# Kernel tuning notes

Hardware: AMD Instinct MI355X
Metric: run time of the kernel (lower is better)

## Reference

```python
import jax, jax.numpy as jnp
import numpy as np

T, B, E, H = 2048, 2, 1024, 16
Dh = E // H


def setup_inputs() -> dict:
    key = jax.random.key(0)
    ks = jax.random.split(key, 5)
    s = 0.02
    query = jax.random.normal(ks[0], (T, B, E), dtype=jnp.float32)
    Wq = jax.random.normal(ks[1], (E, E), dtype=jnp.float32) * s
    Wk = jax.random.normal(ks[2], (E, E), dtype=jnp.float32) * s
    Wv = jax.random.normal(ks[3], (E, E), dtype=jnp.float32) * s
    Wo = jax.random.normal(ks[4], (E, E), dtype=jnp.float32) * s
    bq = jnp.zeros((E,), jnp.float32)
    bk = jnp.zeros((E,), jnp.float32)
    bv = jnp.zeros((E,), jnp.float32)
    bo = jnp.zeros((E,), jnp.float32)
    # additive causal mask: 0 on/below diagonal, -inf above (standard fairseq usage)
    neg = jnp.finfo(jnp.float32).min
    attn_mask = jnp.where(jnp.triu(jnp.ones((T, T), jnp.bool_), k=1), neg, 0.0).astype(jnp.float32)
    return {"query": query, "Wq": Wq, "bq": bq, "Wk": Wk, "bk": bk,
            "Wv": Wv, "bv": bv, "Wo": Wo, "bo": bo, "attn_mask": attn_mask}


def reference(query, Wq, bq, Wk, bk, Wv, bv, Wo, bo, attn_mask):
    t, b, e = query.shape
    scale = Dh ** -0.5
    # self-attention projections (nn.Linear: x @ W.T + b)
    q = (query @ Wq.T + bq) * scale  # [T,B,E]
    k = query @ Wk.T + bk
    v = query @ Wv.T + bv
    # [T, B*H, Dh] -> [B*H, T, Dh]
    q = q.reshape(t, b * H, Dh).transpose(1, 0, 2)
    k = k.reshape(t, b * H, Dh).transpose(1, 0, 2)
    v = v.reshape(t, b * H, Dh).transpose(1, 0, 2)
    # explicit bmm -> softmax -> bmm (materializes [B*H, T, T])
    attn_weights = jnp.einsum('btd,bsd->bts', q, k) + attn_mask[None, :, :]
    attn_probs = jax.nn.softmax(attn_weights, axis=-1)
    attn = jnp.einsum('bts,bsd->btd', attn_probs, v)  # [B*H, T, Dh]
    attn = attn.transpose(1, 0, 2).reshape(t, b, e)  # [T,B,E]
    out = attn @ Wo.T + bo
    return out
```

## Files before the change

kernel.cpp:

```cpp
#include <hip/hip_runtime.h>


typedef __attribute__((ext_vector_type(8))) short   s16x8;
typedef __attribute__((ext_vector_type(4))) float   f32x4;
typedef __attribute__((ext_vector_type(2))) __fp16  f16x2;
typedef __attribute__((ext_vector_type(4))) __fp16  f16x4;

#define MFMA16(a, b, c) __builtin_amdgcn_mfma_f32_16x16x32_bf16((a), (b), (c), 0, 0, 0)
#define MFMApv(a, b, c) __builtin_amdgcn_mfma_f32_16x16x16f16((a), (b), (c), 0, 0, 0)

static __device__ __forceinline__ unsigned short f2bf(float f) {
    unsigned u = __float_as_uint(f);
    unsigned r = u + 0x7fffu + ((u >> 16) & 1u);
    return (unsigned short)(r >> 16);
}

static __device__ __forceinline__ void gl2lds16(const void* g, void* l) {
    __builtin_amdgcn_global_load_lds(
        (const __attribute__((address_space(1))) unsigned int*)g,
        (__attribute__((address_space(3))) unsigned int*)l, 16, 0, 0);
}

__global__ __launch_bounds__(256) void cvt_all(const float* __restrict__ query,
                                               const float* __restrict__ w0,
                                               const float* __restrict__ w1,
                                               const float* __restrict__ w2,
                                               const float* __restrict__ w3,
                                               unsigned short* __restrict__ Xb,
                                               unsigned short* __restrict__ Wcat) {
    const int bx = blockIdx.x;
    if (bx < 4096) {
        const int i = threadIdx.x;
        const float4 f = reinterpret_cast<const float4*>(query + (size_t)bx * 1024)[i];
        ushort4 u;
        u.x = f2bf(f.x); u.y = f2bf(f.y); u.z = f2bf(f.z); u.w = f2bf(f.w);
        const int mrow = (bx & 1) * 2048 + (bx >> 1);
        reinterpret_cast<ushort4*>(Xb + (size_t)mrow * 1024)[i] = u;
    } else {
        const int j   = bx - 4096;
        const int sel = j >> 10;
        const int i   = (j & 1023) * 256 + threadIdx.x;
        const float* src = (sel == 0) ? w0 : (sel == 1) ? w1 : (sel == 2) ? w2 : w3;
        const float4 f = reinterpret_cast<const float4*>(src)[i];
        ushort4 u;
        u.x = f2bf(f.x); u.y = f2bf(f.y); u.z = f2bf(f.z); u.w = f2bf(f.w);
        reinterpret_cast<ushort4*>(Wcat + (size_t)sel * 1048576)[i] = u;
    }
}

__global__ __launch_bounds__(512, 2) void gemm_qkv(const unsigned short* __restrict__ A,
                                                   const unsigned short* __restrict__ W,
                                                   const float* __restrict__ b0,
                                                   const float* __restrict__ b1,
                                                   const float* __restrict__ b2,
                                                   unsigned short* __restrict__ outQK,
                                                   __fp16* __restrict__ outV) {
    __shared__ __align__(16) unsigned short smem[57344];

    const int tid  = threadIdx.x;
    const int w    = tid >> 6;
    const int lane = tid & 63;
    const int quad = lane >> 4;
    const int c    = lane & 15;
    const int wm   = w >> 2;
    const int wn   = w & 3;

    const int id   = blockIdx.x;
    const int xcd  = id & 7;
    const int slot = id >> 3;
    const int m0 = (xcd * 2 + (slot & 1)) * 256;
    const int n0 = (slot >> 1) * 192;

    f32x4 acc[8][3];
    #pragma unroll
    for (int mi = 0; mi < 8; ++mi)
        #pragma unroll
        for (int ni = 0; ni < 3; ++ni) acc[mi][ni] = (f32x4){0.f, 0.f, 0.f, 0.f};

    const int srow = tid >> 3;
    const int g    = (tid & 7) ^ (srow & 7);
    const unsigned short* aG = A + (size_t)(m0 + srow) * 1024 + g * 8;
    const unsigned short* wG = W + (size_t)(n0 + srow) * 1024 + g * 8;
    const int loff = tid * 8;

#define STA(buf, u, k0) gl2lds16(aG + (k0) + (u) * 65536, &smem[(buf) * 28672 + (u) * 4096 + loff])
#define STB(buf, u, k0) gl2lds16(wG + (k0) + (u) * 65536, &smem[(buf) * 28672 + 16384 + (u) * 4096 + loff])

    STB(0, 0, 0); STB(0, 1, 0); STB(0, 2, 0);
    STA(0, 0, 0); STA(0, 2, 0); STA(0, 1, 0); STA(0, 3, 0);
    asm volatile("s_waitcnt vmcnt(2)" ::: "memory");
    asm volatile("s_barrier" ::: "memory");

    const int cs  = c & 7;
    const int ch0 = (quad ^ cs) << 3;
    const int ch1 = ((4 + quad) ^ cs) << 3;

    s16x8 af[4][2], bf[3][2];

    #pragma unroll
    for (int mi = 0; mi < 4; ++mi) {
        const int row = (wm * 128 + mi * 16 + c) * 64;
        af[mi][0] = *reinterpret_cast<const s16x8*>(&smem[row + ch0]);
        af[mi][1] = *reinterpret_cast<const s16x8*>(&smem[row + ch1]);
    }
    #pragma unroll
    for (int ni = 0; ni < 3; ++ni) {
        const int row = (wn * 48 + ni * 16 + c) * 64;
        bf[ni][0] = *reinterpret_cast<const s16x8*>(&smem[16384 + row + ch0]);
        bf[ni][1] = *reinterpret_cast<const s16x8*>(&smem[16384 + row + ch1]);
    }

    #pragma unroll 1
    for (int t = 0; t < 16; ++t) {
        const unsigned short* Al = &smem[(t & 1) * 28672];
        const int  nb   = (t & 1) ^ 1;
        const int  kn   = (t + 1) * 64;
        const bool more = (t < 15);

        if (more) {
            STB(nb, 0, kn); STB(nb, 1, kn); STB(nb, 2, kn);
            STA(nb, 0, kn); STA(nb, 2, kn); STA(nb, 1, kn); STA(nb, 3, kn);
        }

        __builtin_amdgcn_s_setprio(1);
        #pragma unroll
        for (int mi = 0; mi < 4; ++mi)
            #pragma unroll
            for (int ni = 0; ni < 3; ++ni) {
                acc[mi][ni] = MFMA16(af[mi][0], bf[ni][0], acc[mi][ni]);
                acc[mi][ni] = MFMA16(af[mi][1], bf[ni][1], acc[mi][ni]);
            }
        __builtin_amdgcn_s_setprio(0);

        if (more) asm volatile("s_waitcnt vmcnt(7)" ::: "memory");
        else      asm volatile("s_waitcnt vmcnt(0)" ::: "memory");
        asm volatile("s_barrier" ::: "memory");

        #pragma unroll
        for (int mi = 0; mi < 4; ++mi) {
            const int row = (wm * 128 + 64 + mi * 16 + c) * 64;
            af[mi][0] = *reinterpret_cast<const s16x8*>(&Al[row + ch0]);
            af[mi][1] = *reinterpret_cast<const s16x8*>(&Al[row + ch1]);
        }
        __builtin_amdgcn_s_setprio(1);
        #pragma unroll
        for (int mi = 0; mi < 4; ++mi)
            #pragma unroll
            for (int ni = 0; ni < 3; ++ni) {
                acc[4 + mi][ni] = MFMA16(af[mi][0], bf[ni][0], acc[4 + mi][ni]);
                acc[4 + mi][ni] = MFMA16(af[mi][1], bf[ni][1], acc[4 + mi][ni]);
            }
        __builtin_amdgcn_s_setprio(0);

        if (more) {
            asm volatile("s_waitcnt vmcnt(2)" ::: "memory");
            asm volatile("s_barrier" ::: "memory");
            const unsigned short* An = &smem[nb * 28672];
            #pragma unroll
            for (int mi = 0; mi < 4; ++mi) {
                const int row = (wm * 128 + mi * 16 + c) * 64;
                af[mi][0] = *reinterpret_cast<const s16x8*>(&An[row + ch0]);
                af[mi][1] = *reinterpret_cast<const s16x8*>(&An[row + ch1]);
            }
            #pragma unroll
            for (int ni = 0; ni < 3; ++ni) {
                const int row = (wn * 48 + ni * 16 + c) * 64;
                bf[ni][0] = *reinterpret_cast<const s16x8*>(&An[16384 + row + ch0]);
                bf[ni][1] = *reinterpret_cast<const s16x8*>(&An[16384 + row + ch1]);
            }
        }
    }
#undef STA
#undef STB

    const float qs = 0.18033688011112042f;
    #pragma unroll
    for (int ni = 0; ni < 3; ++ni) {
        const int n = n0 + wn * 48 + ni * 16 + c;
        if (n < 2048) {
            const float bval  = (n < 1024) ? b0[n] : b1[n & 1023];
            const float scale = (n < 1024) ? qs : 1.0f;
            #pragma unroll
            for (int mi = 0; mi < 8; ++mi)
                #pragma unroll
                for (int r = 0; r < 4; ++r) {
                    const int m = m0 + wm * 128 + mi * 16 + quad * 4 + r;
                    outQK[(size_t)m * 2048 + n] = f2bf((acc[mi][ni][r] + bval) * scale);
                }
        }
    }

    if (n0 >= 1920) {
        const int vg0 = (n0 >= 2048) ? (n0 - 2048) : 0;
        const int nV  = n0 + 192 - ((n0 > 2048) ? n0 : 2048);
        __fp16* lds16 = reinterpret_cast<__fp16*>(smem);
        __syncthreads();
        #pragma unroll
        for (int ni = 0; ni < 3; ++ni) {
            const int n = n0 + wn * 48 + ni * 16 + c;
            if (n >= 2048) {
                const int lv = (n - 2048) - vg0;
                const float bval = b2[n - 2048];
                #pragma unroll
                for (int mi = 0; mi < 8; ++mi) {
                    const int m = wm * 128 + mi * 16 + quad * 4;
                    const f16x2 lo = __builtin_amdgcn_cvt_pkrtz(acc[mi][ni][0] + bval,
                                                                acc[mi][ni][1] + bval);
                    const f16x2 hi = __builtin_amdgcn_cvt_pkrtz(acc[mi][ni][2] + bval,
                                                                acc[mi][ni][3] + bval);
                    uint2 st;
                    st.x = __builtin_bit_cast(unsigned int, lo);
                    st.y = __builtin_bit_cast(unsigned int, hi);
                    const int phys = lv * 256 + (((m >> 3) ^ (lv & 31)) << 3) + (m & 7);
                    *reinterpret_cast<uint2*>(&lds16[phys]) = st;
                }
            }
        }
        __syncthreads();
        const int lv = tid >> 1;
        if (lv < nV) {
            const int vcol = vg0 + lv;
            const int bb = m0 >> 11, tbase = m0 & 2047;
            __fp16* vdst = outV + ((size_t)((bb * 16 + (vcol >> 6)) * 64 + (vcol & 63))) * 2048 + tbase;
            #pragma unroll
            for (int j = 0; j < 16; ++j) {
                const int lc = (tid & 1) * 16 + j;
                *reinterpret_cast<uint4*>(vdst + lc * 8) =
                    *reinterpret_cast<const uint4*>(&lds16[lv * 256 + ((lc ^ (lv & 31)) << 3)]);
            }
        }
    }
}

__global__ __launch_bounds__(256) void gemm_out(const unsigned short* __restrict__ A,
                                                const unsigned short* __restrict__ W,
                                                const float* __restrict__ bias,
                                                float* __restrict__ outF) {
    __shared__ __align__(16) unsigned short Al[2][64 * 64];
    __shared__ __align__(16) unsigned short Bl[2][128 * 64];

    const int tid  = threadIdx.x;
    const int w    = tid >> 6;
    const int lane = tid & 63;
    const int quad = lane >> 4;
    const int c    = lane & 15;

    const int id   = blockIdx.x;
    const int xcd  = id & 7;
    const int slot = id >> 3;
    const int m0 = (xcd * 8 + (slot & 7)) * 64;
    const int n0 = (slot >> 3) * 128;

    f32x4 acc[8];
    #pragma unroll
    for (int ni = 0; ni < 8; ++ni) acc[ni] = (f32x4){0.f, 0.f, 0.f, 0.f};

    const int srow = tid >> 3;
    const int g    = (tid & 7) ^ (srow & 7);
    const unsigned short* aG = A + (size_t)(m0 + srow) * 1024 + g * 8;
    const unsigned short* wG = W + (size_t)(n0 + srow) * 1024 + g * 8;
    const int loff = tid * 8;

    const int cs = (c & 7);

    gl2lds16(aG,             &Al[0][loff]);
    gl2lds16(aG + 32 * 1024, &Al[0][loff + 2048]);
    #pragma unroll
    for (int i = 0; i < 4; ++i)
        gl2lds16(wG + i * 32 * 1024, &Bl[0][loff + i * 2048]);

    #pragma unroll 1
    for (int kk = 0; kk < 16; ++kk) {
        __syncthreads();
        if (kk < 15) {
            const int k0n = (kk + 1) * 64;
            const int nb  = (kk + 1) & 1;
            gl2lds16(aG + k0n,             &Al[nb][loff]);
            gl2lds16(aG + k0n + 32 * 1024, &Al[nb][loff + 2048]);
            #pragma unroll
            for (int i = 0; i < 4; ++i)
                gl2lds16(wG + k0n + i * 32 * 1024, &Bl[nb][loff + i * 2048]);
        }
        const int cb = kk & 1;
        const int arow = (w * 16 + c) * 64;
        const s16x8 af0 = *reinterpret_cast<const s16x8*>(&Al[cb][arow + ((quad ^ cs) << 3)]);
        const s16x8 af1 = *reinterpret_cast<const s16x8*>(&Al[cb][arow + (((4 + quad) ^ cs) << 3)]);
        __builtin_amdgcn_s_setprio(1);
        #pragma unroll
        for (int ni = 0; ni < 8; ++ni) {
            const int brow = (ni * 16 + c) * 64;
            const s16x8 bf0 = *reinterpret_cast<const s16x8*>(&Bl[cb][brow + ((quad ^ cs) << 3)]);
            const s16x8 bf1 = *reinterpret_cast<const s16x8*>(&Bl[cb][brow + (((4 + quad) ^ cs) << 3)]);
            acc[ni] = MFMA16(af0, bf0, acc[ni]);
            acc[ni] = MFMA16(af1, bf1, acc[ni]);
        }
        __builtin_amdgcn_s_setprio(0);
    }

    #pragma unroll
    for (int ni = 0; ni < 8; ++ni) {
        const int n = n0 + ni * 16 + c;
        const float bval = bias[n];
        const int m = m0 + w * 16 + quad * 4;
        const int bb = m >> 11, t = m & 2047;
        #pragma unroll
        for (int r = 0; r < 4; ++r)
            outF[(size_t)(2 * (t + r) + bb) * 1024 + n] = acc[ni][r] + bval;
    }
}

__global__ __launch_bounds__(256, 4) void attn_kernel(const unsigned short* __restrict__ QKb,
                                                      const __fp16* __restrict__ Vt,
                                                      unsigned short* __restrict__ Ob) {
    __shared__ unsigned short Kl[2][2][64][32];
    __shared__ __fp16 Vl[2][64][64];

    const int tid  = threadIdx.x;
    const int w    = tid >> 6;
    const int lane = tid & 63;
    const int quad = lane >> 4;
    const int c    = lane & 15;

    const int id = blockIdx.x;
    const int bh = (id & 7) * 4 + ((id >> 3) & 3);
    const int kidx = id >> 5;
    const int rr   = kidx >> 3, jj = kidx & 7;
    const int a    = (rr & 1) ? (24 - 8 * rr + jj) : (31 - 8 * rr - jj);
    const int bB = bh >> 4, h = bh & 15;
    const int t0 = a * 64;
    const int trg = t0 + w * 16;
    const int nIt = a + 1;

    const unsigned short* qp = QKb + (size_t)(bB * 2048 + trg + c) * 2048 + h * 64 + quad * 8;
    const s16x8 aq0 = *reinterpret_cast<const s16x8*>(qp);
    const s16x8 aq1 = *reinterpret_cast<const s16x8*>(qp + 32);

    const int lr4 = lane >> 2, sl4 = lane & 3;
    const unsigned short* kSrc = QKb + (size_t)(bB * 2048 + w * 16 + lr4) * 2048
                                 + 1024 + h * 64 + (sl4 ^ ((lane >> 3) & 3)) * 8;
    const int vr8 = lane >> 3, sl8 = lane & 7;
    const __fp16* vSrcA = Vt + (size_t)(bh * 64 + w * 16 + vr8) * 2048 + (sl8 ^ vr8) * 8;
    const __fp16* vSrcB = vSrcA + (size_t)8 * 2048;

    f32x4 acc[4];
    float l = 0.f;
    #pragma unroll
    for (int dt = 0; dt < 4; ++dt) acc[dt] = (f32x4){0.f, 0.f, 0.f, 0.f};

    const int kswz = (quad ^ ((c >> 1) & 3)) * 8;

    {
        gl2lds16(kSrc,      &Kl[0][0][w * 16 + lr4][sl4 * 8]);
        gl2lds16(kSrc + 32, &Kl[0][1][w * 16 + lr4][sl4 * 8]);
        gl2lds16(vSrcA,     &Vl[0][w * 16 + vr8][sl8 * 8]);
        gl2lds16(vSrcB,     &Vl[0][w * 16 + 8 + vr8][sl8 * 8]);
    }

    for (int it = 0; it < nIt; ++it) {
        const int buf = it & 1;
        __syncthreads();
        if (it + 1 < nIt) {
            const size_t s1 = (size_t)(it + 1) * 64;
            const int nb = buf ^ 1;
            gl2lds16(kSrc + s1 * 2048,      &Kl[nb][0][w * 16 + lr4][sl4 * 8]);
            gl2lds16(kSrc + s1 * 2048 + 32, &Kl[nb][1][w * 16 + lr4][sl4 * 8]);
            gl2lds16(vSrcA + s1,            &Vl[nb][w * 16 + vr8][sl8 * 8]);
            gl2lds16(vSrcB + s1,            &Vl[nb][w * 16 + 8 + vr8][sl8 * 8]);
        }

        s16x8 kf[4][2];
        #pragma unroll
        for (int ns = 0; ns < 4; ++ns) {
            kf[ns][0] = *reinterpret_cast<const s16x8*>(&Kl[buf][0][ns * 16 + c][kswz]);
            kf[ns][1] = *reinterpret_cast<const s16x8*>(&Kl[buf][1][ns * 16 + c][kswz]);
        }
        f16x4 vf[4][4];
        #pragma unroll
        for (int dt = 0; dt < 4; ++dt)
            #pragma unroll
            for (int ch = 0; ch < 4; ++ch) {
                const int phys = ((2 * ch + (quad >> 1)) ^ (c & 7)) * 8 + (quad & 1) * 4;
                vf[dt][ch] = *reinterpret_cast<const f16x4*>(&Vl[buf][dt * 16 + c][phys]);
            }

        const int s0 = it * 64;
        const bool diag = (it == a);
        f32x4 sT[4];
        __builtin_amdgcn_s_setprio(1);
        #pragma unroll
        for (int ns = 0; ns < 4; ++ns) {
            f32x4 z = (f32x4){0.f, 0.f, 0.f, 0.f};
            z = MFMA16(kf[ns][0], aq0, z);
            sT[ns] = MFMA16(kf[ns][1], aq1, z);
        }
        __builtin_amdgcn_s_setprio(0);
        f16x4 pf[4];
        float lp = 0.f;
        #pragma unroll
        for (int ns = 0; ns < 4; ++ns) {
            float pv[4];
            #pragma unroll
            for (int r = 0; r < 4; ++r) pv[r] = __builtin_amdgcn_exp2f(sT[ns][r]);
            if (diag) {
                const int sb = s0 + ns * 16 + quad * 4;
                const int qg = trg + c;
                #pragma unroll
                for (int r = 0; r < 4; ++r) if (sb + r > qg) pv[r] = 0.f;
            }
            lp += (pv[0] + pv[1]) + (pv[2] + pv[3]);
            const f16x2 lo = __builtin_amdgcn_cvt_pkrtz(pv[0], pv[1]);
            const f16x2 hi = __builtin_amdgcn_cvt_pkrtz(pv[2], pv[3]);
            pf[ns] = __builtin_shufflevector(lo, hi, 0, 1, 2, 3);
        }
        l += lp;
        __builtin_amdgcn_s_setprio(1);
        #pragma unroll
        for (int dt = 0; dt < 4; ++dt)
            #pragma unroll
            for (int ns = 0; ns < 4; ++ns)
                acc[dt] = MFMApv(vf[dt][ns], pf[ns], acc[dt]);
        __builtin_amdgcn_s_setprio(0);
    }

    float lv = l;
    lv += __shfl_xor(lv, 16);
    lv += __shfl_xor(lv, 32);
    const float inv = 1.0f / lv;
    const size_t base = (size_t)(bB * 2048 + trg + c) * 1024 + h * 64;
    #pragma unroll
    for (int dt = 0; dt < 4; ++dt) {
        const unsigned u0 = (unsigned)f2bf(acc[dt][0] * inv)
                          | ((unsigned)f2bf(acc[dt][1] * inv) << 16);
        const unsigned u1 = (unsigned)f2bf(acc[dt][2] * inv)
                          | ((unsigned)f2bf(acc[dt][3] * inv) << 16);
        uint2 st; st.x = u0; st.y = u1;
        *reinterpret_cast<uint2*>(Ob + base + dt * 16 + quad * 4) = st;
    }
}

extern "C" void kernel_launch(void* const* d_in, const int* in_sizes, int n_in,
                              void* d_out, int out_size, void* d_ws, size_t ws_size,
                              hipStream_t stream) {
    const float* query = (const float*)d_in[0];
    const float* Wq    = (const float*)d_in[1];
    const float* bq    = (const float*)d_in[2];
    const float* Wk    = (const float*)d_in[3];
    const float* bk    = (const float*)d_in[4];
    const float* Wv    = (const float*)d_in[5];
    const float* bv    = (const float*)d_in[6];
    const float* Wo    = (const float*)d_in[7];
    const float* bo    = (const float*)d_in[8];

    float* out = (float*)d_out;

    unsigned short* ws    = (unsigned short*)d_ws;
    unsigned short* Xbf   = ws;
    unsigned short* Wcat  = Xbf  + (size_t)4096 * 1024;
    unsigned short* QKb   = Wcat + (size_t)4 * 1024 * 1024;
    __fp16*         Vtw   = (__fp16*)(QKb + (size_t)4096 * 2048);
    unsigned short* attnb = (unsigned short*)(Vtw + (size_t)32 * 64 * 2048);

    cvt_all<<<8192, 256, 0, stream>>>(query, Wq, Wk, Wv, Wo, Xbf, Wcat);

    gemm_qkv<<<256, 512, 0, stream>>>(Xbf, Wcat, bq, bk, bv, QKb, Vtw);

    attn_kernel<<<1024, 256, 0, stream>>>(QKb, Vtw, attnb);

    gemm_out<<<512, 256, 0, stream>>>(attnb, Wcat + (size_t)3 * 1024 * 1024,
                                      bo, out);
}
```

Baseline: 187.3 us.

## Double query rows per attention block to reuse K/V tiles across two row groups

Each attention block now covers 128 query rows instead of 64, with every wave handling two 16-row groups that share the same K and V fragments loaded from LDS. The grid is halved and launch bounds drop to 2 blocks per SM. The aim is to halve K/V global and LDS traffic per query row and amortise the loop overhead. The cost is more registers per thread (two accumulator sets), lower occupancy, coarser causal work balance, and an extra diagonal tile computed for the first row group.

```diff
diff --git a/kernel.cpp b/kernel.cpp
--- a/kernel.cpp
+++ b/kernel.cpp
@@ -309,7 +309,7 @@
     }
 }
 
-__global__ __launch_bounds__(256, 4) void attn_kernel(const unsigned short* __restrict__ QKb,
+__global__ __launch_bounds__(256, 2) void attn_kernel(const unsigned short* __restrict__ QKb,
                                                       const __fp16* __restrict__ Vt,
                                                       unsigned short* __restrict__ Ob) {
     __shared__ unsigned short Kl[2][2][64][32];
@@ -324,16 +324,18 @@
     const int id = blockIdx.x;
     const int bh = (id & 7) * 4 + ((id >> 3) & 3);
     const int kidx = id >> 5;
-    const int rr   = kidx >> 3, jj = kidx & 7;
-    const int a    = (rr & 1) ? (24 - 8 * rr + jj) : (31 - 8 * rr - jj);
+    const int a    = (kidx < 8) ? (15 - kidx) : (kidx - 8);
     const int bB = bh >> 4, h = bh & 15;
-    const int t0 = a * 64;
-    const int trg = t0 + w * 16;
-    const int nIt = a + 1;
-
-    const unsigned short* qp = QKb + (size_t)(bB * 2048 + trg + c) * 2048 + h * 64 + quad * 8;
-    const s16x8 aq0 = *reinterpret_cast<const s16x8*>(qp);
-    const s16x8 aq1 = *reinterpret_cast<const s16x8*>(qp + 32);
+    const int t0 = a * 128;
+    const int trg = t0 + w * 32;
+    const int nIt = 2 * a + 2;
+
+    const unsigned short* qp0 = QKb + (size_t)(bB * 2048 + trg + c) * 2048 + h * 64 + quad * 8;
+    const s16x8 aq0 = *reinterpret_cast<const s16x8*>(qp0);
+    const s16x8 aq1 = *reinterpret_cast<const s16x8*>(qp0 + 32);
+    const unsigned short* qp1 = qp0 + (size_t)16 * 2048;
+    const s16x8 aq2 = *reinterpret_cast<const s16x8*>(qp1);
+    const s16x8 aq3 = *reinterpret_cast<const s16x8*>(qp1 + 32);
 
     const int lr4 = lane >> 2, sl4 = lane & 3;
     const unsigned short* kSrc = QKb + (size_t)(bB * 2048 + w * 16 + lr4) * 2048
@@ -342,10 +344,13 @@
     const __fp16* vSrcA = Vt + (size_t)(bh * 64 + w * 16 + vr8) * 2048 + (sl8 ^ vr8) * 8;
     const __fp16* vSrcB = vSrcA + (size_t)8 * 2048;
 
-    f32x4 acc[4];
-    float l = 0.f;
-    #pragma unroll
-    for (int dt = 0; dt < 4; ++dt) acc[dt] = (f32x4){0.f, 0.f, 0.f, 0.f};
+    f32x4 acc0[4], acc1[4];
+    float l0 = 0.f, l1 = 0.f;
+    #pragma unroll
+    for (int dt = 0; dt < 4; ++dt) {
+        acc0[dt] = (f32x4){0.f, 0.f, 0.f, 0.f};
+        acc1[dt] = (f32x4){0.f, 0.f, 0.f, 0.f};
+    }
 
     const int kswz = (quad ^ ((c >> 1) & 3)) * 8;
 
@@ -384,7 +389,7 @@
             }
 
         const int s0 = it * 64;
-        const bool diag = (it == a);
+
         f32x4 sT[4];
         __builtin_amdgcn_s_setprio(1);
         #pragma unroll
@@ -394,47 +399,96 @@
             sT[ns] = MFMA16(kf[ns][1], aq1, z);
         }
         __builtin_amdgcn_s_setprio(0);
-        f16x4 pf[4];
-        float lp = 0.f;
+        f16x4 pf0[4];
+        {
+            const bool dg = (s0 + 63 > trg);
+            float lp = 0.f;
+            #pragma unroll
+            for (int ns = 0; ns < 4; ++ns) {
+                float pv[4];
+                #pragma unroll
+                for (int r = 0; r < 4; ++r) pv[r] = __builtin_amdgcn_exp2f(sT[ns][r]);
+                if (dg) {
+                    const int sb = s0 + ns * 16 + quad * 4;
+                    const int qg = trg + c;
+                    #pragma unroll
+                    for (int r = 0; r < 4; ++r) if (sb + r > qg) pv[r] = 0.f;
+                }
+                lp += (pv[0] + pv[1]) + (pv[2] + pv[3]);
+                const f16x2 lo = __builtin_amdgcn_cvt_pkrtz(pv[0], pv[1]);
+                const f16x2 hi = __builtin_amdgcn_cvt_pkrtz(pv[2], pv[3]);
+                pf0[ns] = __builtin_shufflevector(lo, hi, 0, 1, 2, 3);
+            }
+            l0 += lp;
+        }
+
+        __builtin_amdgcn_s_setprio(1);
         #pragma unroll
         for (int ns = 0; ns < 4; ++ns) {
-            float pv[4];
-            #pragma unroll
-            for (int r = 0; r < 4; ++r) pv[r] = __builtin_amdgcn_exp2f(sT[ns][r]);
-            if (diag) {
-                const int sb = s0 + ns * 16 + quad * 4;
-                const int qg = trg + c;
+            f32x4 z = (f32x4){0.f, 0.f, 0.f, 0.f};
+            z = MFMA16(kf[ns][0], aq2, z);
+            sT[ns] = MFMA16(kf[ns][1], aq3, z);
+        }
+        __builtin_amdgcn_s_setprio(0);
+        f16x4 pf1[4];
+        {
+            const bool dg = (s0 + 63 > trg + 16);
+            float lp = 0.f;
+            #pragma unroll
+            for (int ns = 0; ns < 4; ++ns) {
+                float pv[4];
                 #pragma unroll
-                for (int r = 0; r < 4; ++r) if (sb + r > qg) pv[r] = 0.f;
-            }
-            lp += (pv[0] + pv[1]) + (pv[2] + pv[3]);
-            const f16x2 lo = __builtin_amdgcn_cvt_pkrtz(pv[0], pv[1]);
-            const f16x2 hi = __builtin_amdgcn_cvt_pkrtz(pv[2], pv[3]);
-            pf[ns] = __builtin_shufflevector(lo, hi, 0, 1, 2, 3);
-        }
-        l += lp;
+                for (int r = 0; r < 4; ++r) pv[r] = __builtin_amdgcn_exp2f(sT[ns][r]);
+                if (dg) {
+                    const int sb = s0 + ns * 16 + quad * 4;
+                    const int qg = trg + 16 + c;
+                    #pragma unroll
+                    for (int r = 0; r < 4; ++r) if (sb + r > qg) pv[r] = 0.f;
+                }
+                lp += (pv[0] + pv[1]) + (pv[2] + pv[3]);
+                const f16x2 lo = __builtin_amdgcn_cvt_pkrtz(pv[0], pv[1]);
+                const f16x2 hi = __builtin_amdgcn_cvt_pkrtz(pv[2], pv[3]);
+                pf1[ns] = __builtin_shufflevector(lo, hi, 0, 1, 2, 3);
+            }
+            l1 += lp;
+        }
+
         __builtin_amdgcn_s_setprio(1);
         #pragma unroll
         for (int dt = 0; dt < 4; ++dt)
             #pragma unroll
-            for (int ns = 0; ns < 4; ++ns)
-                acc[dt] = MFMApv(vf[dt][ns], pf[ns], acc[dt]);
+            for (int ns = 0; ns < 4; ++ns) {
+                acc0[dt] = MFMApv(vf[dt][ns], pf0[ns], acc0[dt]);
+                acc1[dt] = MFMApv(vf[dt][ns], pf1[ns], acc1[dt]);
+            }
         __builtin_amdgcn_s_setprio(0);
     }
 
-    float lv = l;
-    lv += __shfl_xor(lv, 16);
-    lv += __shfl_xor(lv, 32);
-    const float inv = 1.0f / lv;
-    const size_t base = (size_t)(bB * 2048 + trg + c) * 1024 + h * 64;
+    float lv0 = l0;
+    lv0 += __shfl_xor(lv0, 16);
+    lv0 += __shfl_xor(lv0, 32);
+    const float inv0 = 1.0f / lv0;
+    float lv1 = l1;
+    lv1 += __shfl_xor(lv1, 16);
+    lv1 += __shfl_xor(lv1, 32);
+    const float inv1 = 1.0f / lv1;
+
+    const size_t base0 = (size_t)(bB * 2048 + trg + c) * 1024 + h * 64;
+    const size_t base1 = base0 + (size_t)16 * 1024;
     #pragma unroll
     for (int dt = 0; dt < 4; ++dt) {
-        const unsigned u0 = (unsigned)f2bf(acc[dt][0] * inv)
-                          | ((unsigned)f2bf(acc[dt][1] * inv) << 16);
-        const unsigned u1 = (unsigned)f2bf(acc[dt][2] * inv)
-                          | ((unsigned)f2bf(acc[dt][3] * inv) << 16);
+        unsigned u0 = (unsigned)f2bf(acc0[dt][0] * inv0)
+                    | ((unsigned)f2bf(acc0[dt][1] * inv0) << 16);
+        unsigned u1 = (unsigned)f2bf(acc0[dt][2] * inv0)
+                    | ((unsigned)f2bf(acc0[dt][3] * inv0) << 16);
         uint2 st; st.x = u0; st.y = u1;
-        *reinterpret_cast<uint2*>(Ob + base + dt * 16 + quad * 4) = st;
+        *reinterpret_cast<uint2*>(Ob + base0 + dt * 16 + quad * 4) = st;
+        u0 = (unsigned)f2bf(acc1[dt][0] * inv1)
+           | ((unsigned)f2bf(acc1[dt][1] * inv1) << 16);
+        u1 = (unsigned)f2bf(acc1[dt][2] * inv1)
+           | ((unsigned)f2bf(acc1[dt][3] * inv1) << 16);
+        uint2 st2; st2.x = u0; st2.y = u1;
+        *reinterpret_cast<uint2*>(Ob + base1 + dt * 16 + quad * 4) = st2;
     }
 }
 
@@ -464,7 +518,7 @@
 
     gemm_qkv<<<256, 512, 0, stream>>>(Xbf, Wcat, bq, bk, bv, QKb, Vtw);
 
-    attn_kernel<<<1024, 256, 0, stream>>>(QKb, Vtw, attnb);
+    attn_kernel<<<512, 256, 0, stream>>>(QKb, Vtw, attnb);
 
     gemm_out<<<512, 256, 0, stream>>>(attnb, Wcat + (size_t)3 * 1024 * 1024,
                                       bo, out);
```

After: 205.6 us. +9.8%, slower.

## Split long causal attention rows across key chunks with a combine kernel

Applied to the files above, without the earlier changes.

Long query tiles now have their key range split into 2-4 chunks, each handled by a separate block, giving 2560 blocks instead of 1024 and work that is more evenly sized. Chunks write unnormalized fp32 partial outputs and row sums to workspace, and a new combine kernel adds them and normalizes. The aim is to remove the causal tail imbalance where a few blocks run many iterations. The cost is extra global traffic for the partials, plus an additional kernel launch. The split relies on a fixed max rather than per-chunk max tracking, as the original already did.

```diff
diff --git a/kernel.cpp b/kernel.cpp
--- a/kernel.cpp
+++ b/kernel.cpp
@@ -311,7 +311,9 @@
 
 __global__ __launch_bounds__(256, 4) void attn_kernel(const unsigned short* __restrict__ QKb,
                                                       const __fp16* __restrict__ Vt,
-                                                      unsigned short* __restrict__ Ob) {
+                                                      unsigned short* __restrict__ Ob,
+                                                      float* __restrict__ Po,
+                                                      float* __restrict__ Pl) {
     __shared__ unsigned short Kl[2][2][64][32];
     __shared__ __fp16 Vl[2][64][64];
 
@@ -322,14 +324,23 @@
     const int c    = lane & 15;
 
     const int id = blockIdx.x;
-    const int bh = (id & 7) * 4 + ((id >> 3) & 3);
-    const int kidx = id >> 5;
-    const int rr   = kidx >> 3, jj = kidx & 7;
-    const int a    = (rr & 1) ? (24 - 8 * rr + jj) : (31 - 8 * rr - jj);
+    const int bh = id & 31;
+    const int e  = 79 - (id >> 5);
+    int a, ci, nc;
+    if (e < 8)       { a = e;                ci = 0;          nc = 1; }
+    else if (e < 24) { const int k = e - 8;  a = 8 + (k >> 1);  ci = k & 1;      nc = 2; }
+    else if (e < 48) { const int k = e - 24; const int q3 = (k * 11) >> 5;
+                       a = 16 + q3;          ci = k - 3 * q3;  nc = 3; }
+    else             { const int k = e - 48; a = 24 + (k >> 2); ci = k & 3;      nc = 4; }
+    const int U = a + 1;
+    int u0, u1;
+    if (nc == 1)      { u0 = 0;                  u1 = U; }
+    else if (nc == 2) { u0 = (ci * U) >> 1;      u1 = ((ci + 1) * U) >> 1; }
+    else if (nc == 3) { u0 = (ci * U * 11) >> 5; u1 = ((ci + 1) * U * 11) >> 5; }
+    else              { u0 = (ci * U) >> 2;      u1 = ((ci + 1) * U) >> 2; }
+
     const int bB = bh >> 4, h = bh & 15;
-    const int t0 = a * 64;
-    const int trg = t0 + w * 16;
-    const int nIt = a + 1;
+    const int trg = a * 64 + w * 16;
 
     const unsigned short* qp = QKb + (size_t)(bB * 2048 + trg + c) * 2048 + h * 64 + quad * 8;
     const s16x8 aq0 = *reinterpret_cast<const s16x8*>(qp);
@@ -350,16 +361,18 @@
     const int kswz = (quad ^ ((c >> 1) & 3)) * 8;
 
     {
-        gl2lds16(kSrc,      &Kl[0][0][w * 16 + lr4][sl4 * 8]);
-        gl2lds16(kSrc + 32, &Kl[0][1][w * 16 + lr4][sl4 * 8]);
-        gl2lds16(vSrcA,     &Vl[0][w * 16 + vr8][sl8 * 8]);
-        gl2lds16(vSrcB,     &Vl[0][w * 16 + 8 + vr8][sl8 * 8]);
-    }
-
-    for (int it = 0; it < nIt; ++it) {
+        const size_t s0r = (size_t)u0 * 64;
+        const int b0 = u0 & 1;
+        gl2lds16(kSrc + s0r * 2048,      &Kl[b0][0][w * 16 + lr4][sl4 * 8]);
+        gl2lds16(kSrc + s0r * 2048 + 32, &Kl[b0][1][w * 16 + lr4][sl4 * 8]);
+        gl2lds16(vSrcA + s0r,            &Vl[b0][w * 16 + vr8][sl8 * 8]);
+        gl2lds16(vSrcB + s0r,            &Vl[b0][w * 16 + 8 + vr8][sl8 * 8]);
+    }
+
+    for (int it = u0; it < u1; ++it) {
         const int buf = it & 1;
         __syncthreads();
-        if (it + 1 < nIt) {
+        if (it + 1 < u1) {
             const size_t s1 = (size_t)(it + 1) * 64;
             const int nb = buf ^ 1;
             gl2lds16(kSrc + s1 * 2048,      &Kl[nb][0][w * 16 + lr4][sl4 * 8]);
@@ -425,16 +438,70 @@
     float lv = l;
     lv += __shfl_xor(lv, 16);
     lv += __shfl_xor(lv, 32);
-    const float inv = 1.0f / lv;
-    const size_t base = (size_t)(bB * 2048 + trg + c) * 1024 + h * 64;
-    #pragma unroll
-    for (int dt = 0; dt < 4; ++dt) {
-        const unsigned u0 = (unsigned)f2bf(acc[dt][0] * inv)
-                          | ((unsigned)f2bf(acc[dt][1] * inv) << 16);
-        const unsigned u1 = (unsigned)f2bf(acc[dt][2] * inv)
-                          | ((unsigned)f2bf(acc[dt][3] * inv) << 16);
-        uint2 st; st.x = u0; st.y = u1;
-        *reinterpret_cast<uint2*>(Ob + base + dt * 16 + quad * 4) = st;
+
+    if (nc == 1) {
+        const float inv = 1.0f / lv;
+        const size_t base = (size_t)(bB * 2048 + trg + c) * 1024 + h * 64;
+        #pragma unroll
+        for (int dt = 0; dt < 4; ++dt) {
+            const unsigned u0b = (unsigned)f2bf(acc[dt][0] * inv)
+                               | ((unsigned)f2bf(acc[dt][1] * inv) << 16);
+            const unsigned u1b = (unsigned)f2bf(acc[dt][2] * inv)
+                               | ((unsigned)f2bf(acc[dt][3] * inv) << 16);
+            uint2 st; st.x = u0b; st.y = u1b;
+            *reinterpret_cast<uint2*>(Ob + base + dt * 16 + quad * 4) = st;
+        }
+    } else {
+        const int slot = (bh * 32 + a) * 4 + ci;
+        float* po = Po + (size_t)slot * 4096 + (w * 16 + c) * 64 + quad * 4;
+        #pragma unroll
+        for (int dt = 0; dt < 4; ++dt) {
+            float4 st;
+            st.x = acc[dt][0]; st.y = acc[dt][1]; st.z = acc[dt][2]; st.w = acc[dt][3];
+            *reinterpret_cast<float4*>(po + dt * 16) = st;
+        }
+        if (quad == 0) Pl[(size_t)slot * 64 + w * 16 + c] = lv;
+    }
+}
+
+__global__ __launch_bounds__(256) void attn_combine(const float* __restrict__ Po,
+                                                    const float* __restrict__ Pl,
+                                                    unsigned short* __restrict__ Ob) {
+    const int id = blockIdx.x;
+    const int bh = id & 31;
+    const int a  = 8 + (id >> 5);
+    const int nc = (a < 16) ? 2 : (a < 24) ? 3 : 4;
+    const int bB = bh >> 4, h = bh & 15;
+
+    const int tid = threadIdx.x;
+    const int q   = tid >> 2;
+    const int ds  = (tid & 3) * 16;
+
+    const int slot0 = (bh * 32 + a) * 4;
+
+    float lsum = 0.f;
+    for (int ci = 0; ci < nc; ++ci) lsum += Pl[(size_t)(slot0 + ci) * 64 + q];
+    const float inv = 1.0f / lsum;
+
+    float4 o[4];
+    #pragma unroll
+    for (int j = 0; j < 4; ++j) o[j] = (float4){0.f, 0.f, 0.f, 0.f};
+    for (int ci = 0; ci < nc; ++ci) {
+        const float* p = Po + (size_t)(slot0 + ci) * 4096 + q * 64 + ds;
+        #pragma unroll
+        for (int j = 0; j < 4; ++j) {
+            const float4 v = reinterpret_cast<const float4*>(p)[j];
+            o[j].x += v.x; o[j].y += v.y; o[j].z += v.z; o[j].w += v.w;
+        }
+    }
+
+    unsigned short* dst = Ob + (size_t)(bB * 2048 + a * 64 + q) * 1024 + h * 64 + ds;
+    #pragma unroll
+    for (int j = 0; j < 4; ++j) {
+        uint2 st;
+        st.x = (unsigned)f2bf(o[j].x * inv) | ((unsigned)f2bf(o[j].y * inv) << 16);
+        st.y = (unsigned)f2bf(o[j].z * inv) | ((unsigned)f2bf(o[j].w * inv) << 16);
+        *reinterpret_cast<uint2*>(dst + j * 4) = st;
     }
 }
 
@@ -459,12 +526,16 @@
     unsigned short* QKb   = Wcat + (size_t)4 * 1024 * 1024;
     __fp16*         Vtw   = (__fp16*)(QKb + (size_t)4096 * 2048);
     unsigned short* attnb = (unsigned short*)(Vtw + (size_t)32 * 64 * 2048);
+    float*          Pob   = (float*)(attnb + (size_t)4096 * 1024);
+    float*          Plb   = Pob + (size_t)4096 * 4096;
 
     cvt_all<<<8192, 256, 0, stream>>>(query, Wq, Wk, Wv, Wo, Xbf, Wcat);
 
     gemm_qkv<<<256, 512, 0, stream>>>(Xbf, Wcat, bq, bk, bv, QKb, Vtw);
 
-    attn_kernel<<<1024, 256, 0, stream>>>(QKb, Vtw, attnb);
+    attn_kernel<<<2560, 256, 0, stream>>>(QKb, Vtw, attnb, Pob, Plb);
+
+    attn_combine<<<768, 256, 0, stream>>>(Pob, Plb, attnb);
 
     gemm_out<<<512, 256, 0, stream>>>(attnb, Wcat + (size_t)3 * 1024 * 1024,
                                       bo, out);
```

Result: slower. 195.4 us (+4.3%).
